# Optimization experiments

Measured on AMD Instinct MI355X. Metric: run time of the kernel, lower is better.

Reference implementation:

```python
import jax, jax.numpy as jnp
import numpy as np

HID = 1152      # vision_hidden_size
HEADS = 16      # vision_num_heads
HD = HID // HEADS  # 72
INTER = 4304    # vision_intermediate_size
SEQ = 16384     # total vision tokens
WIN = 64        # tokens per attention window
EPS = 1e-6


def setup_inputs() -> dict:
    key = jax.random.key(0)
    ks = jax.random.split(key, 14)
    f32 = jnp.float32
    x = jax.random.normal(ks[0], (SEQ, HID), f32)
    # RoPE tables: standard rotary angles, full head_dim via concat(ang, ang)
    inv_freq = 1.0 / (10000.0 ** (jnp.arange(0, HD // 2, dtype=f32) / (HD // 2)))
    ang = jnp.arange(SEQ, dtype=f32)[:, None] * inv_freq[None, :]
    emb = jnp.concatenate([ang, ang], axis=-1)          # [SEQ, HD]
    cos, sin = jnp.cos(emb), jnp.sin(emb)
    cu_seqlens = jnp.arange(SEQ // WIN + 1, dtype=jnp.int32) * WIN  # uniform windows
    sc = 0.02
    return {
        "x": x, "cos": cos, "sin": sin, "cu_seqlens": cu_seqlens,
        "qkv_w": jax.random.normal(ks[1], (HID, 3 * HID), f32) * sc,
        "qkv_b": jnp.zeros((3 * HID,), f32),
        "proj_w": jax.random.normal(ks[2], (HID, HID), f32) * sc,
        "proj_b": jnp.zeros((HID,), f32),
        "ln1_w": jnp.ones((HID,), f32), "ln1_b": jnp.zeros((HID,), f32),
        "ln2_w": jnp.ones((HID,), f32), "ln2_b": jnp.zeros((HID,), f32),
        "fc1_w": jax.random.normal(ks[3], (HID, INTER), f32) * sc,
        "fc1_b": jnp.zeros((INTER,), f32),
        "fc2_w": jax.random.normal(ks[4], (INTER, HID), f32) * sc,
        "fc2_b": jnp.zeros((HID,), f32),
    }


def _layer_norm(h, w, b):
    hf = h.astype(jnp.float32)
    mean = jnp.mean(hf, axis=-1, keepdims=True)
    var = jnp.mean((hf - mean) ** 2, axis=-1, keepdims=True)
    return ((hf - mean) * jax.lax.rsqrt(var + EPS)) * w + b


def _rotate_half(t):
    t1, t2 = jnp.split(t, 2, axis=-1)
    return jnp.concatenate((-t2, t1), axis=-1)


def reference(x, cos, sin, cu_seqlens,
              qkv_w, qkv_b, proj_w, proj_b,
              ln1_w, ln1_b, ln2_w, ln2_b,
              fc1_w, fc1_b, fc2_w, fc2_b):
    S = x.shape[0]
    n_win = cu_seqlens.shape[0] - 1
    W = S // n_win  # uniform windows (block-diagonal attention)

    # --- attention branch ---
    h = _layer_norm(x, ln1_w, ln1_b)
    qkv = h @ qkv_w + qkv_b
    q, k, v = jnp.split(qkv, 3, axis=-1)
    q = q.reshape(S, HEADS, HD)
    k = k.reshape(S, HEADS, HD)
    v = v.reshape(S, HEADS, HD)
    c = cos[:, None, :HD]
    s = sin[:, None, :HD]
    q = q * c + _rotate_half(q) * s
    k = k * c + _rotate_half(k) * s
    # block-diagonal windowed attention: [n_win, W, HEADS, HD]
    qw = q.reshape(n_win, W, HEADS, HD).astype(jnp.float32)
    kw = k.reshape(n_win, W, HEADS, HD).astype(jnp.float32)
    vw = v.reshape(n_win, W, HEADS, HD).astype(jnp.float32)
    scores = jnp.einsum('wqhd,wkhd->whqk', qw, kw) * (HD ** -0.5)
    probs = jax.nn.softmax(scores, axis=-1)
    out = jnp.einsum('whqk,wkhd->wqhd', probs, vw).reshape(S, HID)
    x = x + (out @ proj_w + proj_b)

    # --- MLP branch ---
    h2 = _layer_norm(x, ln2_w, ln2_b)
    m = jax.nn.gelu(h2 @ fc1_w + fc1_b, approximate=True)
    return x + (m @ fc2_w + fc2_b)
```

## Files before the change

### kernel.cpp

```cpp
#include <hip/hip_runtime.h>
#include <stdint.h>


#define SEQ   16384
#define HID   1152
#define NH    16
#define HDIM  72
#define INTER 4304
#define INTERP 4352
#define QKVN  3456

using bf16x8 = __attribute__((ext_vector_type(8))) __bf16;
using f32x4  = __attribute__((ext_vector_type(4))) float;

__device__ __forceinline__ float bf2f(uint16_t u){ return __uint_as_float(((uint32_t)u)<<16); }
__device__ __forceinline__ uint16_t f2bf(float f){
  uint32_t u = __float_as_uint(f);
  u += 0x7fffu + ((u>>16)&1u);
  return (uint16_t)(u>>16);
}
__device__ __forceinline__ float gelu_tanh(float x){
  float t = tanhf(0.7978845608028654f*(x + 0.044715f*x*x*x));
  return 0.5f*x*(1.0f + t);
}
__device__ __forceinline__ void async_load16(const void* g, void* l){
  __builtin_amdgcn_global_load_lds((__attribute__((address_space(1))) void*)(void*)g,
                                   (__attribute__((address_space(3))) void*)l, 16, 0, 0);
}

__global__ void transpose_cast(const float* __restrict__ src, uint16_t* __restrict__ dst,
                               int R, int C, int Rp)
{
  __shared__ float tile[32][33];
  const int tx = threadIdx.x & 31, ty = threadIdx.x >> 5;
  const int c = blockIdx.x*32 + tx;
  #pragma unroll
  for (int s = 0; s < 4; ++s){
    const int r = blockIdx.y*32 + ty + s*8;
    tile[ty + s*8][tx] = (r < R && c < C) ? src[(size_t)r*C + c] : 0.0f;
  }
  __syncthreads();
  #pragma unroll
  for (int s = 0; s < 4; ++s){
    const int oc = blockIdx.x*32 + ty + s*8;
    const int orr = blockIdx.y*32 + tx;
    dst[(size_t)oc*Rp + orr] = f2bf(tile[tx][ty + s*8]);
  }
}

__global__ void ln_kernel(const float* __restrict__ x, const float* __restrict__ w,
                          const float* __restrict__ b, uint16_t* __restrict__ out)
{
  const int wid = threadIdx.x >> 6, lane = threadIdx.x & 63;
  const int row = blockIdx.x*4 + wid;
  const float* xr = x + (size_t)row*HID;
  float v[18];
  float s = 0.f;
  #pragma unroll
  for (int t = 0; t < 18; ++t){ v[t] = xr[lane + t*64]; s += v[t]; }
  #pragma unroll
  for (int m = 32; m; m >>= 1) s += __shfl_xor(s, m, 64);
  const float mean = s * (1.0f/HID);
  float q = 0.f;
  #pragma unroll
  for (int t = 0; t < 18; ++t){ float d = v[t]-mean; q += d*d; }
  #pragma unroll
  for (int m = 32; m; m >>= 1) q += __shfl_xor(q, m, 64);
  const float rstd = rsqrtf(q*(1.0f/HID) + 1e-6f);
  uint16_t* orow = out + (size_t)row*HID;
  #pragma unroll
  for (int t = 0; t < 18; ++t){
    const int j = lane + t*64;
    orow[j] = f2bf((v[t]-mean)*rstd*w[j] + b[j]);
  }
}

__global__ void rope_kernel(uint16_t* __restrict__ qkv, const float* __restrict__ cosb,
                            const float* __restrict__ sinb)
{
  const int idx = blockIdx.x*256 + threadIdx.x;
  const int s  = idx / (NH*18);
  const int r1 = idx - s*(NH*18);
  const int h  = r1 / 18;
  const int d2 = (r1 - h*18)*2;
  const float2 c  = *(const float2*)(cosb + s*HDIM + d2);
  const float2 sn = *(const float2*)(sinb + s*HDIM + d2);
  const size_t b = (size_t)s*QKVN + h*HDIM + d2;
  uint32_t* p = (uint32_t*)(qkv + b);
  {
    uint32_t lo = p[0], hi = p[18];
    float x0 = bf2f((uint16_t)lo), x1 = bf2f((uint16_t)(lo>>16));
    float y0 = bf2f((uint16_t)hi), y1 = bf2f((uint16_t)(hi>>16));
    p[0]  = (uint32_t)f2bf(x0*c.x - y0*sn.x) | ((uint32_t)f2bf(x1*c.y - y1*sn.y) << 16);
    p[18] = (uint32_t)f2bf(y0*c.x + x0*sn.x) | ((uint32_t)f2bf(y1*c.y + x1*sn.y) << 16);
  }
  {
    uint32_t lo = p[HID/2], hi = p[HID/2 + 18];
    float x0 = bf2f((uint16_t)lo), x1 = bf2f((uint16_t)(lo>>16));
    float y0 = bf2f((uint16_t)hi), y1 = bf2f((uint16_t)(hi>>16));
    p[HID/2]      = (uint32_t)f2bf(x0*c.x - y0*sn.x) | ((uint32_t)f2bf(x1*c.y - y1*sn.y) << 16);
    p[HID/2 + 18] = (uint32_t)f2bf(y0*c.x + x0*sn.x) | ((uint32_t)f2bf(y1*c.y + x1*sn.y) << 16);
  }
}

__global__ __launch_bounds__(256,2) void attn_kernel(const uint16_t* __restrict__ qkv,
                                                     uint16_t* __restrict__ outb)
{
  __shared__ float Q[64*76];
  __shared__ float K[64*76];
  __shared__ float V[64*76];
  __shared__ float P[64*68];
  const int tid = threadIdx.x;
  const int win = blockIdx.x >> 4, h = blockIdx.x & 15;
  const size_t base = (size_t)win*64*QKVN + h*HDIM;
  {
    const int r = tid >> 2, q4 = tid & 3;
    const size_t rb = base + (size_t)r*QKVN;
    #pragma unroll
    for (int p0 = 0; p0 < 9; ++p0){
      const int p = q4*9 + p0;
      const uint32_t uq = *(const uint32_t*)(qkv + rb + 2*p);
      const uint32_t uk = *(const uint32_t*)(qkv + rb + HID + 2*p);
      const uint32_t uv = *(const uint32_t*)(qkv + rb + 2*HID + 2*p);
      Q[r*76+2*p] = bf2f((uint16_t)uq); Q[r*76+2*p+1] = bf2f((uint16_t)(uq>>16));
      K[r*76+2*p] = bf2f((uint16_t)uk); K[r*76+2*p+1] = bf2f((uint16_t)(uk>>16));
      V[r*76+2*p] = bf2f((uint16_t)uv); V[r*76+2*p+1] = bf2f((uint16_t)(uv>>16));
    }
  }
  __syncthreads();
  const int rg = tid >> 4, cg = tid & 15;
  const int r0 = rg*4, c0 = cg*4;
  float sc[4][4] = {};
  #pragma unroll 3
  for (int kk = 0; kk < 18; ++kk){
    float4 qv[4], kv[4];
    #pragma unroll
    for (int i = 0; i < 4; ++i) qv[i] = *(const float4*)&Q[(r0+i)*76 + kk*4];
    #pragma unroll
    for (int j = 0; j < 4; ++j) kv[j] = *(const float4*)&K[(c0+j)*76 + kk*4];
    #pragma unroll
    for (int i = 0; i < 4; ++i)
      #pragma unroll
      for (int j = 0; j < 4; ++j)
        sc[i][j] += qv[i].x*kv[j].x + qv[i].y*kv[j].y + qv[i].z*kv[j].z + qv[i].w*kv[j].w;
  }
  const float scale = 0.11785113019775793f;
  #pragma unroll
  for (int i = 0; i < 4; ++i){
    float a0 = sc[i][0]*scale, a1 = sc[i][1]*scale, a2 = sc[i][2]*scale, a3 = sc[i][3]*scale;
    float m = fmaxf(fmaxf(a0,a1), fmaxf(a2,a3));
    m = fmaxf(m, __shfl_xor(m, 1, 16));
    m = fmaxf(m, __shfl_xor(m, 2, 16));
    m = fmaxf(m, __shfl_xor(m, 4, 16));
    m = fmaxf(m, __shfl_xor(m, 8, 16));
    float e0 = __expf(a0-m), e1 = __expf(a1-m), e2 = __expf(a2-m), e3 = __expf(a3-m);
    float sm = e0+e1+e2+e3;
    sm += __shfl_xor(sm, 1, 16);
    sm += __shfl_xor(sm, 2, 16);
    sm += __shfl_xor(sm, 4, 16);
    sm += __shfl_xor(sm, 8, 16);
    const float inv = 1.0f/sm;
    *(float4*)&P[(r0+i)*68 + c0] = make_float4(e0*inv, e1*inv, e2*inv, e3*inv);
  }
  __syncthreads();
  for (int d4 = cg; d4 < 18; d4 += 16){
    float4 o[4] = {};
    #pragma unroll 4
    for (int k4 = 0; k4 < 16; ++k4){
      float4 pr[4];
      #pragma unroll
      for (int i = 0; i < 4; ++i) pr[i] = *(const float4*)&P[(r0+i)*68 + k4*4];
      const float4 v0 = *(const float4*)&V[(k4*4+0)*76 + d4*4];
      const float4 v1 = *(const float4*)&V[(k4*4+1)*76 + d4*4];
      const float4 v2 = *(const float4*)&V[(k4*4+2)*76 + d4*4];
      const float4 v3 = *(const float4*)&V[(k4*4+3)*76 + d4*4];
      #pragma unroll
      for (int i = 0; i < 4; ++i){
        o[i].x += pr[i].x*v0.x + pr[i].y*v1.x + pr[i].z*v2.x + pr[i].w*v3.x;
        o[i].y += pr[i].x*v0.y + pr[i].y*v1.y + pr[i].z*v2.y + pr[i].w*v3.y;
        o[i].z += pr[i].x*v0.z + pr[i].y*v1.z + pr[i].z*v2.z + pr[i].w*v3.z;
        o[i].w += pr[i].x*v0.w + pr[i].y*v1.w + pr[i].z*v2.w + pr[i].w*v3.w;
      }
    }
    #pragma unroll
    for (int i = 0; i < 4; ++i){
      const int token = win*64 + r0 + i;
      const size_t ob = (size_t)token*HID + h*HDIM + d4*4;
      outb[ob+0] = f2bf(o[i].x); outb[ob+1] = f2bf(o[i].y);
      outb[ob+2] = f2bf(o[i].z); outb[ob+3] = f2bf(o[i].w);
    }
  }
}

template<int EPI>
__global__ __launch_bounds__(256,4) void gemm_bt(
    const uint16_t* __restrict__ A, const uint16_t* __restrict__ Bt,
    const float* __restrict__ bias, int Nb,
    const float* res, void* outp, int N, int K, int NB)
{
  __shared__ uint16_t sA[128*32];
  __shared__ uint16_t sB[128*32];
  const int tid = threadIdx.x, wid = tid >> 6, lane = tid & 63;
  const int per  = gridDim.x >> 3;
  const int tile = (blockIdx.x & 7)*per + (blockIdx.x >> 3);
  const int mb   = tile / NB;
  const int mBase = mb*128, nBase = (tile - mb*NB)*128;
  const int wm = wid >> 1, wn = wid & 1;

  const int srow = tid >> 2;
  const int g    = (tid & 3) ^ ((srow >> 1) & 3);
  const uint16_t* pa0 = A  + (size_t)(mBase + srow)*K      + g*8;
  const uint16_t* pa1 = A  + (size_t)(mBase + 64 + srow)*K + g*8;
  const uint16_t* pb0 = Bt + (size_t)(nBase + srow)*K      + g*8;
  const uint16_t* pb1 = Bt + (size_t)(nBase + 64 + srow)*K + g*8;
  uint16_t* dstA0 = sA + wid*512;
  uint16_t* dstA1 = sA + 2048 + wid*512;
  uint16_t* dstB0 = sB + wid*512;
  uint16_t* dstB1 = sB + 2048 + wid*512;

  const int rl16 = lane & 15, kg = lane >> 4;
  const int phys = kg ^ ((rl16 >> 1) & 3);
  int offA[4], offB[4];
  #pragma unroll
  for (int i = 0; i < 4; ++i){
    offA[i] = (wm*64 + i*16 + rl16)*32 + phys*8;
    offB[i] = (wn*64 + i*16 + rl16)*32 + phys*8;
  }

  f32x4 acc[4][4] = {};

  for (int k0 = 0; k0 < K; k0 += 32){
    __syncthreads();
    async_load16(pa0 + k0, dstA0);
    async_load16(pa1 + k0, dstA1);
    async_load16(pb0 + k0, dstB0);
    async_load16(pb1 + k0, dstB1);
    __syncthreads();
    bf16x8 af[4], bfr[4];
    #pragma unroll
    for (int i = 0; i < 4; ++i) af[i]  = *(const bf16x8*)&sA[offA[i]];
    #pragma unroll
    for (int j = 0; j < 4; ++j) bfr[j] = *(const bf16x8*)&sB[offB[j]];
    #pragma unroll
    for (int i = 0; i < 4; ++i)
      #pragma unroll
      for (int j = 0; j < 4; ++j)
        acc[i][j] = __builtin_amdgcn_mfma_f32_16x16x32_bf16(af[i], bfr[j], acc[i][j], 0, 0, 0);
  }

  const int rqd = (lane>>4)*4, cl = lane & 15;
  #pragma unroll
  for (int i = 0; i < 4; ++i){
    #pragma unroll
    for (int j = 0; j < 4; ++j){
      const int col = nBase + wn*64 + j*16 + cl;
      const float bv = (col < Nb) ? bias[col] : 0.0f;
      #pragma unroll
      for (int r = 0; r < 4; ++r){
        const int row = mBase + wm*64 + i*16 + rqd + r;
        const float v = acc[i][j][r] + bv;
        const size_t o = (size_t)row*N + col;
        if (EPI == 0)      ((uint16_t*)outp)[o] = f2bf(v);
        else if (EPI == 1) ((uint16_t*)outp)[o] = f2bf(gelu_tanh(v));
        else               ((float*)outp)[o] = v + res[o];
      }
    }
  }
}

extern "C" void kernel_launch(void* const* d_in, const int* in_sizes, int n_in,
                              void* d_out, int out_size, void* d_ws, size_t ws_size,
                              hipStream_t stream)
{
  const float* x      = (const float*)d_in[0];
  const float* cosb   = (const float*)d_in[1];
  const float* sinb   = (const float*)d_in[2];
  const float* qkv_w  = (const float*)d_in[4];
  const float* qkv_b  = (const float*)d_in[5];
  const float* proj_w = (const float*)d_in[6];
  const float* proj_b = (const float*)d_in[7];
  const float* ln1_w  = (const float*)d_in[8];
  const float* ln1_b  = (const float*)d_in[9];
  const float* ln2_w  = (const float*)d_in[10];
  const float* ln2_b  = (const float*)d_in[11];
  const float* fc1_w  = (const float*)d_in[12];
  const float* fc1_b  = (const float*)d_in[13];
  const float* fc2_w  = (const float*)d_in[14];
  const float* fc2_b  = (const float*)d_in[15];

  char* ws = (char*)d_ws;
  uint16_t* Wqkv  = (uint16_t*)(ws + 0);
  uint16_t* Wproj = (uint16_t*)(ws + 7962624);
  uint16_t* Wfc1  = (uint16_t*)(ws + 10616832);
  uint16_t* Wfc2  = (uint16_t*)(ws + 20643840);
  uint16_t* Hbuf  = (uint16_t*)(ws + 30670848);
  uint16_t* QKV   = (uint16_t*)(ws + 68419584);
  uint16_t* MB    = QKV;
  float* X1 = (float*)d_out;

  transpose_cast<<<dim3(108,36), 256, 0, stream>>>(qkv_w, Wqkv, 1152, 3456, 1152);
  transpose_cast<<<dim3(36,36),  256, 0, stream>>>(proj_w, Wproj, 1152, 1152, 1152);
  transpose_cast<<<dim3(136,36), 256, 0, stream>>>(fc1_w, Wfc1, 1152, 4304, 1152);
  transpose_cast<<<dim3(36,136), 256, 0, stream>>>(fc2_w, Wfc2, 4304, 1152, 4352);

  ln_kernel<<<4096, 256, 0, stream>>>(x, ln1_w, ln1_b, Hbuf);
  gemm_bt<0><<<27*128, 256, 0, stream>>>(Hbuf, Wqkv, qkv_b, QKVN, nullptr, QKV, QKVN, HID, 27);
  rope_kernel<<<18432, 256, 0, stream>>>(QKV, cosb, sinb);
  attn_kernel<<<4096, 256, 0, stream>>>(QKV, Hbuf);
  gemm_bt<2><<<9*128, 256, 0, stream>>>(Hbuf, Wproj, proj_b, HID, x, X1, HID, HID, 9);
  ln_kernel<<<4096, 256, 0, stream>>>(X1, ln2_w, ln2_b, Hbuf);
  gemm_bt<1><<<34*128, 256, 0, stream>>>(Hbuf, Wfc1, fc1_b, INTER, nullptr, MB, INTERP, HID, 34);
  gemm_bt<2><<<9*128, 256, 0, stream>>>(MB, Wfc2, fc2_b, HID, X1, X1, HID, INTERP, 9);
}
```

Measured before the change: 1.214 ms.

## Double-buffer GEMM LDS tiles with async prefetch and partial waitcnt

Doubles the shared-memory tiles in the bf16 GEMM so the global-to-LDS async loads for the next K-step are issued before the MFMAs of the current step. Raw s_barrier and explicit vmcnt waits (leaving 4 loads in flight) replace the two __syncthreads per iteration. The aim is to hide global memory latency behind compute. LDS usage per block doubles, which may reduce occupancy. The hand-written waitcnt encodings and barriers are also fragile with respect to LDS read/write ordering.

```diff
diff --git a/kernel.cpp b/kernel.cpp
--- a/kernel.cpp
+++ b/kernel.cpp
@@ -26,6 +26,9 @@
 __device__ __forceinline__ void async_load16(const void* g, void* l){
   __builtin_amdgcn_global_load_lds((__attribute__((address_space(1))) void*)(void*)g,
                                    (__attribute__((address_space(3))) void*)l, 16, 0, 0);
+}
+__device__ __forceinline__ void raw_barrier(){
+  __asm__ volatile("s_barrier" ::: "memory");
 }
 
 __global__ void transpose_cast(const float* __restrict__ src, uint16_t* __restrict__ dst,
@@ -198,8 +201,8 @@
     const float* __restrict__ bias, int Nb,
     const float* res, void* outp, int N, int K, int NB)
 {
-  __shared__ uint16_t sA[128*32];
-  __shared__ uint16_t sB[128*32];
+  __shared__ uint16_t sA[2*4096];
+  __shared__ uint16_t sB[2*4096];
   const int tid = threadIdx.x, wid = tid >> 6, lane = tid & 63;
   const int per  = gridDim.x >> 3;
   const int tile = (blockIdx.x & 7)*per + (blockIdx.x >> 3);
@@ -213,10 +216,7 @@
   const uint16_t* pa1 = A  + (size_t)(mBase + 64 + srow)*K + g*8;
   const uint16_t* pb0 = Bt + (size_t)(nBase + srow)*K      + g*8;
   const uint16_t* pb1 = Bt + (size_t)(nBase + 64 + srow)*K + g*8;
-  uint16_t* dstA0 = sA + wid*512;
-  uint16_t* dstA1 = sA + 2048 + wid*512;
-  uint16_t* dstB0 = sB + wid*512;
-  uint16_t* dstB1 = sB + 2048 + wid*512;
+  const int d0 = wid*512, d1 = 2048 + wid*512;
 
   const int rl16 = lane & 15, kg = lane >> 4;
   const int phys = kg ^ ((rl16 >> 1) & 3);
@@ -228,19 +228,31 @@
   }
 
   f32x4 acc[4][4] = {};
-
-  for (int k0 = 0; k0 < K; k0 += 32){
-    __syncthreads();
-    async_load16(pa0 + k0, dstA0);
-    async_load16(pa1 + k0, dstA1);
-    async_load16(pb0 + k0, dstB0);
-    async_load16(pb1 + k0, dstB1);
-    __syncthreads();
+  const int NI = K >> 5;
+
+  async_load16(pa0, sA + d0); async_load16(pa1, sA + d1);
+  async_load16(pb0, sB + d0); async_load16(pb1, sB + d1);
+
+  for (int it = 0; it < NI; ++it){
+    const int cur = it & 1;
+    raw_barrier();
+    if (it + 1 < NI){
+      const int k0 = (it + 1) << 5;
+      const int bo = (cur ^ 1) * 4096;
+      async_load16(pa0 + k0, sA + bo + d0); async_load16(pa1 + k0, sA + bo + d1);
+      async_load16(pb0 + k0, sB + bo + d0); async_load16(pb1 + k0, sB + bo + d1);
+      __builtin_amdgcn_s_waitcnt(0x0F74);
+    } else {
+      __builtin_amdgcn_s_waitcnt(0x0F70);
+    }
+    raw_barrier();
+    const uint16_t* bA = sA + cur*4096;
+    const uint16_t* bB = sB + cur*4096;
     bf16x8 af[4], bfr[4];
     #pragma unroll
-    for (int i = 0; i < 4; ++i) af[i]  = *(const bf16x8*)&sA[offA[i]];
-    #pragma unroll
-    for (int j = 0; j < 4; ++j) bfr[j] = *(const bf16x8*)&sB[offB[j]];
+    for (int i = 0; i < 4; ++i) af[i]  = *(const bf16x8*)&bA[offA[i]];
+    #pragma unroll
+    for (int j = 0; j < 4; ++j) bfr[j] = *(const bf16x8*)&bB[offB[j]];
     #pragma unroll
     for (int i = 0; i < 4; ++i)
       #pragma unroll
```

Result: no change. 1.222 ms (+0.6%).
